# Kernel tuning notes

Hardware: AMD Instinct MI355X
Metric: run time of the kernel (lower is better)

The kernel has to match this reference:

```python
import jax, jax.numpy as jnp
import numpy as np

B, C, H, W = 16, 3, 224, 224
P = 16
DIM = 256
NL = 8
DS = 16          # d_state (mamba default)
DCONV = 4
NCLS = 1000
DI = 2 * DIM     # expand * dim
DTR = -(-DIM // 16)  # dt_rank = ceil(dim/16)
NPATCH = (H // P) * (W // P)
SEQ = NPATCH + 1


def _ln(x, g, b, eps=1e-5):
    mu = x.mean(-1, keepdims=True)
    var = ((x - mu) ** 2).mean(-1, keepdims=True)
    return (x - mu) * jax.lax.rsqrt(var + eps) * g + b


def setup_inputs() -> dict:
    key = jax.random.key(0)
    ks = jax.random.split(key, 12)
    pd = C * P * P
    s = 0.02
    return dict(
        img=jax.random.normal(ks[0], (B, C, H, W), jnp.float32),
        pe_ln1_g=jnp.ones((pd,), jnp.float32), pe_ln1_b=jnp.zeros((pd,), jnp.float32),
        pe_w=jax.random.normal(ks[1], (pd, DIM), jnp.float32) * s,
        pe_b=jnp.zeros((DIM,), jnp.float32),
        pe_ln2_g=jnp.ones((DIM,), jnp.float32), pe_ln2_b=jnp.zeros((DIM,), jnp.float32),
        pos_emb=jax.random.normal(ks[2], (1, SEQ, DIM), jnp.float32) * s,
        cls_tok=jax.random.normal(ks[3], (1, 1, DIM), jnp.float32) * s,
        ln_w=jnp.ones((NL, DIM), jnp.float32), ln_b=jnp.zeros((NL, DIM), jnp.float32),
        in_w=jax.random.normal(ks[4], (NL, DIM, 2 * DI), jnp.float32) * s,
        conv_w=jax.random.normal(ks[5], (NL, DI, DCONV), jnp.float32) * s,
        conv_b=jnp.zeros((NL, DI), jnp.float32),
        xproj_w=jax.random.normal(ks[6], (NL, DI, DTR + 2 * DS), jnp.float32) * s,
        dtproj_w=jax.random.normal(ks[7], (NL, DTR, DI), jnp.float32) * s,
        dtproj_b=jax.random.uniform(ks[8], (NL, DI), jnp.float32, -4.0, -2.0),
        A_log=jnp.log(jnp.broadcast_to(jnp.arange(1, DS + 1, dtype=jnp.float32), (NL, DI, DS))) + jnp.zeros((NL, DI, DS), jnp.float32),
        Dp=jnp.ones((NL, DI), jnp.float32),
        out_w=jax.random.normal(ks[9], (NL, DI, DIM), jnp.float32) * s,
        normf_w=jnp.ones((DIM,), jnp.float32), normf_b=jnp.zeros((DIM,), jnp.float32),
        head_w=jax.random.normal(ks[10], (DIM, NCLS), jnp.float32) * s,
        head_b=jnp.zeros((NCLS,), jnp.float32),
    )


def _mamba(x, in_w, conv_w, conv_b, xproj_w, dtproj_w, dtproj_b, A_log, Dp, out_w):
    b, L, _ = x.shape
    xz = x @ in_w                       # (b, L, 2*DI)
    xm, z = jnp.split(xz, 2, axis=-1)
    # causal depthwise conv1d (torch pads both sides then slices -> left-pad d_conv-1)
    xc = jnp.pad(xm.transpose(0, 2, 1), ((0, 0), (0, 0), (DCONV - 1, 0)))
    xc = jax.lax.conv_general_dilated(
        xc, conv_w[:, None, :], (1,), 'VALID',
        dimension_numbers=('NCH', 'OIH', 'NCH'), feature_group_count=DI)
    u = jax.nn.silu(xc + conv_b[None, :, None]).transpose(0, 2, 1)  # (b, L, DI)
    dbc = u @ xproj_w                   # (b, L, DTR+2*DS)
    dt, Bm, Cm = jnp.split(dbc, [DTR, DTR + DS], axis=-1)
    dt = jax.nn.softplus(dt @ dtproj_w + dtproj_b)  # (b, L, DI)
    A = -jnp.exp(A_log)                 # (DI, DS)

    def step(h, inp):
        dt_t, B_t, C_t, u_t = inp       # (b,DI), (b,DS), (b,DS), (b,DI)
        dA = jnp.exp(dt_t[:, :, None] * A)                 # (b, DI, DS)
        h = dA * h + (dt_t * u_t)[:, :, None] * B_t[:, None, :]
        y = jnp.einsum('bdn,bn->bd', h, C_t)
        return h, y

    h0 = jnp.zeros((b, DI, DS), x.dtype)
    xs = (dt.transpose(1, 0, 2), Bm.transpose(1, 0, 2),
          Cm.transpose(1, 0, 2), u.transpose(1, 0, 2))
    _, ys = jax.lax.scan(step, h0, xs)
    y = ys.transpose(1, 0, 2) + u * Dp  # (b, L, DI)
    y = y * jax.nn.silu(z)
    return y @ out_w                    # (b, L, DIM)


def reference(img, pe_ln1_g, pe_ln1_b, pe_w, pe_b, pe_ln2_g, pe_ln2_b, pos_emb,
              cls_tok, ln_w, ln_b, in_w, conv_w, conv_b, xproj_w, dtproj_w,
              dtproj_b, A_log, Dp, out_w, normf_w, normf_b, head_w, head_b):
    b = img.shape[0]
    h, w = H // P, W // P
    # 'b c (h p1) (w p2) -> b (h w) (p1 p2 c)'
    x = img.reshape(b, C, h, P, w, P).transpose(0, 2, 4, 3, 5, 1).reshape(b, h * w, P * P * C)
    x = _ln(x, pe_ln1_g, pe_ln1_b)
    x = x @ pe_w + pe_b
    x = _ln(x, pe_ln2_g, pe_ln2_b)
    x = jnp.concatenate([jnp.broadcast_to(cls_tok, (b, 1, DIM)), x], axis=1)
    x = x + pos_emb[:, :x.shape[1]]
    residual = None
    for i in range(NL):
        residual = x if residual is None else x + residual
        xn = _ln(residual, ln_w[i], ln_b[i])
        x = _mamba(xn, in_w[i], conv_w[i], conv_b[i], xproj_w[i],
                   dtproj_w[i], dtproj_b[i], A_log[i], Dp[i], out_w[i])
    residual = x + residual
    x = _ln(residual, normf_w, normf_b)
    x = x[:, 0]                          # pool == 'cls'
    return x @ head_w + head_b
```

## Files before the change

kernel.cpp:

```cpp
#include <hip/hip_runtime.h>
#include <math.h>

#define NB   16
#define SEQL 197
#define TB   (NB*SEQL)
#define DIMM 256
#define DI   512
#define DS   16
#define NL   8

typedef __bf16 bf16x8 __attribute__((ext_vector_type(8)));
typedef __bf16 bf16x4 __attribute__((ext_vector_type(4)));
typedef float floatx4 __attribute__((ext_vector_type(4)));

__device__ __forceinline__ void block_reduce_2(float& s1, float& s2, float* red, int tid){
  #pragma unroll
  for (int off = 32; off > 0; off >>= 1){
    s1 += __shfl_down(s1, off, 64);
    s2 += __shfl_down(s2, off, 64);
  }
  __syncthreads();
  if ((tid & 63) == 0){ red[(tid>>6)*2] = s1; red[(tid>>6)*2+1] = s2; }
  __syncthreads();
  s1 = red[0] + red[2] + red[4] + red[6];
  s2 = red[1] + red[3] + red[5] + red[7];
}

__global__ __launch_bounds__(256) void prep_weights(
    const float* __restrict__ in_w, const float* __restrict__ out_w,
    const float* __restrict__ pe_w, const float* __restrict__ xproj,
    __bf16* __restrict__ wt_in, __bf16* __restrict__ wt_out,
    __bf16* __restrict__ wt_pe, float* __restrict__ wt_xp_f)
{
  __shared__ float t[32][33];
  int bid = blockIdx.x;
  const float* src; __bf16* dst = nullptr; float* dstf = nullptr;
  int K, Nin, n0, k0;
  if (bid < 2048){
    int z = bid >> 8, tt = bid & 255;
    K = 256; Nin = 1024; n0 = (tt & 31)*32; k0 = (tt >> 5)*32;
    src = in_w  + (size_t)z*K*Nin;
    dst = wt_in + (size_t)z*K*Nin;
  } else if (bid < 3072){
    int t2 = bid - 2048; int z = t2 >> 7, tt = t2 & 127;
    K = 512; Nin = 256; n0 = (tt & 7)*32; k0 = (tt >> 3)*32;
    src = out_w  + (size_t)z*K*Nin;
    dst = wt_out + (size_t)z*K*Nin;
  } else if (bid < 3264){
    int tt = bid - 3072;
    K = 768; Nin = 256; n0 = (tt & 7)*32; k0 = (tt >> 3)*32;
    src = pe_w; dst = wt_pe;
  } else {
    int t2 = bid - 3264; int z = t2 >> 5, tt = t2 & 31;
    K = 512; Nin = 48; n0 = (tt & 1)*32; k0 = (tt >> 1)*32;
    src  = xproj + (size_t)z*K*Nin;
    dstf = wt_xp_f + (size_t)z*64*512;
  }
  int tx = threadIdx.x & 31, ty = threadIdx.x >> 5;
  #pragma unroll
  for (int j = 0; j < 4; j++){
    int n = n0 + tx;
    t[ty + j*8][tx] = (n < Nin) ? src[(size_t)(k0 + ty + j*8)*Nin + n] : 0.f;
  }
  __syncthreads();
  if (dstf){
    #pragma unroll
    for (int j = 0; j < 4; j++){
      int k = k0 + tx, c = n0 + ty + j*8;
      dstf[(size_t)(k>>2)*256 + c*4 + (k&3)] = t[tx][ty + j*8];
    }
  } else {
    #pragma unroll
    for (int j = 0; j < 4; j++)
      dst[(size_t)(n0 + ty + j*8)*K + k0 + tx] = (__bf16)t[tx][ty + j*8];
  }
}

template<int BM, int BN, int KS>
__global__ __launch_bounds__(256) void gemm_bf16(
    const __bf16* __restrict__ A, const __bf16* __restrict__ Wt,
    const float* __restrict__ bias, float* __restrict__ C, int M, int N, int K)
{
  constexpr int BK  = 32;
  constexpr int LDA = BK + 8;
  constexpr int TMW = BM/32;
  constexpr int TNW = BN/32;
  __shared__ __bf16 As[BM][LDA];
  __shared__ __bf16 Bs[BN][LDA];

  int tid  = threadIdx.x;
  int lane = tid & 63, w = tid >> 6;
  int wm = w >> 1, wn = w & 1;
  int l15 = lane & 15, quad = lane >> 4;
  int nt = blockIdx.x / KS, ks = blockIdx.x % KS;
  int bm = blockIdx.y * BM, bn = nt * BN;
  int kbeg = ks * (K / KS), kend = kbeg + (K / KS);

  floatx4 acc[TMW][TNW] = {};

  for (int k0 = kbeg; k0 < kend; k0 += BK){
    #pragma unroll
    for (int i = 0; i < BM/64; i++){
      int c = tid + i*256;
      int row = c >> 2, kc = c & 3;
      int m = bm + row;
      uint4 v = make_uint4(0,0,0,0);
      if (m < M) v = ((const uint4*)(A + (size_t)m*K + k0))[kc];
      *(uint4*)&As[row][kc*8] = v;
    }
    #pragma unroll
    for (int i = 0; i < BN/64; i++){
      int c = tid + i*256;
      int row = c >> 2, kc = c & 3;
      int n = bn + row;
      uint4 v = ((const uint4*)(Wt + (size_t)n*K + k0))[kc];
      *(uint4*)&Bs[row][kc*8] = v;
    }
    __syncthreads();
    bf16x8 af[TMW], bf[TNW];
    #pragma unroll
    for (int mi = 0; mi < TMW; mi++)
      af[mi] = *(const bf16x8*)&As[wm*(BM/2) + mi*16 + l15][quad*8];
    #pragma unroll
    for (int ni = 0; ni < TNW; ni++)
      bf[ni] = *(const bf16x8*)&Bs[wn*(BN/2) + ni*16 + l15][quad*8];
    #pragma unroll
    for (int mi = 0; mi < TMW; mi++)
      #pragma unroll
      for (int ni = 0; ni < TNW; ni++)
        acc[mi][ni] = __builtin_amdgcn_mfma_f32_16x16x32_bf16(af[mi], bf[ni], acc[mi][ni], 0, 0, 0);
    __syncthreads();
  }
  #pragma unroll
  for (int mi = 0; mi < TMW; mi++){
    #pragma unroll
    for (int ni = 0; ni < TNW; ni++){
      int col = bn + wn*(BN/2) + ni*16 + l15;
      float bv = (KS == 1 && bias) ? bias[col] : 0.f;
      #pragma unroll
      for (int r = 0; r < 4; r++){
        int row = bm + wm*(BM/2) + mi*16 + quad*4 + r;
        if (row < M){
          if (KS == 1) C[(size_t)row*N + col] = acc[mi][ni][r] + bv;
          else         atomicAdd(&C[(size_t)row*N + col], acc[mi][ni][r]);
        }
      }
    }
  }
}

template<int DO_LN>
__global__ __launch_bounds__(512) void gemm_out_fused(
    const __bf16* __restrict__ A, const __bf16* __restrict__ Wt,
    float* __restrict__ resid, __bf16* __restrict__ xn_bf,
    const float* __restrict__ g, const float* __restrict__ bta)
{
  constexpr int BK = 64, LDA = BK + 8;
  __shared__ alignas(16) char smem[(16 + 256) * LDA * sizeof(__bf16)];
  __bf16 (*As)[LDA] = (__bf16(*)[LDA])smem;
  __bf16 (*Bs)[LDA] = (__bf16(*)[LDA])(smem + 16*LDA*sizeof(__bf16));
  float  (*sy)[264] = (float(*)[264])smem;

  int tid = threadIdx.x, lane = tid & 63, w = tid >> 6;
  int l15 = lane & 15, quad = lane >> 4;
  int bm = blockIdx.x * 16;

  floatx4 acc[2] = {};
  for (int k0 = 0; k0 < 512; k0 += BK){
    if (tid < 128){
      int row = tid >> 3, kc = tid & 7;
      *(uint4*)&As[row][kc*8] = ((const uint4*)(A + (size_t)(bm+row)*512 + k0))[kc];
    }
    #pragma unroll
    for (int i = 0; i < 4; i++){
      int c = tid + i*512;
      int row = c >> 3, kc = c & 7;
      *(uint4*)&Bs[row][kc*8] = ((const uint4*)(Wt + (size_t)row*512 + k0))[kc];
    }
    __syncthreads();
    #pragma unroll
    for (int kk = 0; kk < 2; kk++){
      bf16x8 af = *(const bf16x8*)&As[l15][kk*32 + quad*8];
      #pragma unroll
      for (int ni = 0; ni < 2; ni++){
        bf16x8 bfv = *(const bf16x8*)&Bs[w*32 + ni*16 + l15][kk*32 + quad*8];
        acc[ni] = __builtin_amdgcn_mfma_f32_16x16x32_bf16(af, bfv, acc[ni], 0, 0, 0);
      }
    }
    __syncthreads();
  }
  #pragma unroll
  for (int ni = 0; ni < 2; ni++){
    int col = w*32 + ni*16 + l15;
    #pragma unroll
    for (int r = 0; r < 4; r++)
      sy[quad*4 + r][col] = acc[ni][r];
  }
  __syncthreads();
  #pragma unroll
  for (int rr = 0; rr < 2; rr++){
    int row = w*2 + rr;
    size_t base = (size_t)(bm + row)*256 + lane*4;
    float4 y4 = *(const float4*)&sy[row][lane*4];
    float4 rv = *(const float4*)&resid[base];
    float4 v;
    v.x = y4.x + rv.x; v.y = y4.y + rv.y; v.z = y4.z + rv.z; v.w = y4.w + rv.w;
    *(float4*)&resid[base] = v;
    if (DO_LN){
      float s  = v.x + v.y + v.z + v.w;
      float s2 = v.x*v.x + v.y*v.y + v.z*v.z + v.w*v.w;
      #pragma unroll
      for (int off = 1; off < 64; off <<= 1){
        s  += __shfl_xor(s,  off, 64);
        s2 += __shfl_xor(s2, off, 64);
      }
      float mu  = s * (1.f/256.f);
      float var = s2 * (1.f/256.f) - mu*mu;
      float rrq = rsqrtf(var + 1e-5f);
      float4 gv = *(const float4*)&g[lane*4];
      float4 bv = *(const float4*)&bta[lane*4];
      bf16x4 o;
      o[0] = (__bf16)((v.x - mu)*rrq*gv.x + bv.x);
      o[1] = (__bf16)((v.y - mu)*rrq*gv.y + bv.y);
      o[2] = (__bf16)((v.z - mu)*rrq*gv.z + bv.z);
      o[3] = (__bf16)((v.w - mu)*rrq*gv.w + bv.w);
      *(bf16x4*)&xn_bf[base] = o;
    }
  }
}

__global__ __launch_bounds__(256) void patch_ln1(
    const float* __restrict__ img, const float* __restrict__ g1, const float* __restrict__ b1,
    __bf16* __restrict__ xp_bf)
{
  __shared__ float red[8];
  int blk = blockIdx.x;
  int b = blk / 196, p = blk % 196;
  int hh = p / 14, ww = p % 14;
  int tid = threadIdx.x;

  float v[3]; float s = 0.f, s2 = 0.f;
  #pragma unroll
  for (int i = 0; i < 3; i++){
    int e  = tid + i*256;
    int c  = e % 3;
    int p2 = (e/3) % 16;
    int p1 = e / 48;
    float val = img[((b*3 + c)*224 + hh*16 + p1)*224 + ww*16 + p2];
    v[i] = val; s += val; s2 += val*val;
  }
  block_reduce_2(s, s2, red, tid);
  float mu = s * (1.f/768.f);
  float var = s2 * (1.f/768.f) - mu*mu;
  float rr = rsqrtf(var + 1e-5f);
  #pragma unroll
  for (int i = 0; i < 3; i++){
    int e = tid + i*256;
    xp_bf[(size_t)blk*768 + e] = (__bf16)((v[i] - mu) * rr * g1[e] + b1[e]);
  }
}

__global__ __launch_bounds__(256) void ln2_cls_pos(
    const float* __restrict__ pemb, const float* __restrict__ g2, const float* __restrict__ b2,
    const float* __restrict__ pos, const float* __restrict__ cls,
    float* __restrict__ resid,
    const float* __restrict__ g0, const float* __restrict__ b0,
    __bf16* __restrict__ xn_bf)
{
  __shared__ float red[8];
  int blk = blockIdx.x;
  int b = blk / SEQL, l = blk % SEQL;
  int tid = threadIdx.x;
  float o;
  if (l == 0){
    o = cls[tid] + pos[tid];
  } else {
    int p = l - 1;
    float v = pemb[(size_t)(b*196 + p)*256 + tid];
    float s = v, s2 = v*v;
    block_reduce_2(s, s2, red, tid);
    float mu = s * (1.f/256.f);
    float var = s2 * (1.f/256.f) - mu*mu;
    float rr = rsqrtf(var + 1e-5f);
    o = (v - mu) * rr * g2[tid] + b2[tid] + pos[l*256 + tid];
  }
  size_t idx = (size_t)blk*256 + tid;
  resid[idx] = o;
  float s = o, s2 = o*o;
  block_reduce_2(s, s2, red, tid);
  float mu = s * (1.f/256.f);
  float var = s2 * (1.f/256.f) - mu*mu;
  float rr = rsqrtf(var + 1e-5f);
  xn_bf[idx] = (__bf16)((o - mu) * rr * g0[tid] + b0[tid]);
}

__global__ __launch_bounds__(256) void conv_xproj(
    const float* __restrict__ xz, const float* __restrict__ cw, const float* __restrict__ cb,
    const float* __restrict__ wxp,
    float* __restrict__ u, float* __restrict__ dbc)
{
  __shared__ float s_u[8][512];
  __shared__ float s_acc[4][8][64];
  int tid = threadIdx.x;
  int t0 = blockIdx.x * 8;

  int d = (tid & 127) * 4;
  float4 w0 = *(const float4*)&cw[(d+0)*4];
  float4 w1 = *(const float4*)&cw[(d+1)*4];
  float4 w2 = *(const float4*)&cw[(d+2)*4];
  float4 w3 = *(const float4*)&cw[(d+3)*4];
  float4 cbv = *(const float4*)&cb[d];
  const float4 z4 = make_float4(0.f,0.f,0.f,0.f);
  #pragma unroll
  for (int j = 0; j < 4; j++){
    int tl = (tid >> 7)*4 + j;
    int t = t0 + tl;
    int l = t % SEQL;
    float4 x0 = *(const float4*)&xz[(size_t)t*1024 + d];
    float4 x1 = (l>=1) ? *(const float4*)&xz[(size_t)(t-1)*1024 + d] : z4;
    float4 x2 = (l>=2) ? *(const float4*)&xz[(size_t)(t-2)*1024 + d] : z4;
    float4 x3 = (l>=3) ? *(const float4*)&xz[(size_t)(t-3)*1024 + d] : z4;
    float4 r = cbv;
    r.x += x3.x*w0.x + x2.x*w0.y + x1.x*w0.z + x0.x*w0.w;
    r.y += x3.y*w1.x + x2.y*w1.y + x1.y*w1.z + x0.y*w1.w;
    r.z += x3.z*w2.x + x2.z*w2.y + x1.z*w2.z + x0.z*w2.w;
    r.w += x3.w*w3.x + x2.w*w3.y + x1.w*w3.z + x0.w*w3.w;
    r.x *= 1.f/(1.f + __expf(-r.x));
    r.y *= 1.f/(1.f + __expf(-r.y));
    r.z *= 1.f/(1.f + __expf(-r.z));
    r.w *= 1.f/(1.f + __expf(-r.w));
    *(float4*)&u[(size_t)t*512 + d] = r;
    *(float4*)&s_u[tl][d] = r;
  }
  __syncthreads();

  int col = tid & 63, sl = tid >> 6;
  const float4* wp4 = (const float4*)wxp + (size_t)sl*32*64 + col;
  float a[8] = {};
  #pragma unroll 4
  for (int k4 = 0; k4 < 32; k4++){
    float4 wv = wp4[(size_t)k4*64];
    #pragma unroll
    for (int t = 0; t < 8; t++){
      float4 v = *(const float4*)&s_u[t][sl*128 + k4*4];
      a[t] += wv.x*v.x + wv.y*v.y + wv.z*v.z + wv.w*v.w;
    }
  }
  #pragma unroll
  for (int t = 0; t < 8; t++) s_acc[sl][t][col] = a[t];
  __syncthreads();
  #pragma unroll
  for (int j = 0; j < 2; j++){
    int p = tid + j*256;
    int tok = p >> 6, c2 = p & 63;
    if (c2 < 48){
      float v = s_acc[0][tok][c2] + s_acc[1][tok][c2]
              + s_acc[2][tok][c2] + s_acc[3][tok][c2];
      dbc[(size_t)(t0 + tok)*64 + c2] = v;
    }
  }
}

#define SCT 32
#define NCH ((SEQL + SCT - 1)/SCT)
#define NDL 8
__global__ __launch_bounds__(128) void scan_kernel(
    const float* __restrict__ u, const float* __restrict__ dbc,
    const float* __restrict__ xz, const float* __restrict__ A_log, const float* __restrict__ Dp,
    const float* __restrict__ dtw, const float* __restrict__ dtb,
    __bf16* __restrict__ yg_bf)
{
  __shared__ float s_D [16][36];
  __shared__ float s_B [16][36];
  __shared__ float s_C [16][36];
  __shared__ float s_u [NDL][36];
  __shared__ float s_z [NDL][36];
  __shared__ float s_dt[NDL][36];
  __shared__ float s_yp[SCT][NDL][20];
  __shared__ float s_dp[NDL];

  int tid = threadIdx.x;
  int n = tid & 15, dl = tid >> 4;
  int b = blockIdx.x >> 6, dg = blockIdx.x & 63;
  int d0 = dg * NDL;
  const size_t base = (size_t)b * SEQL;

  float A = -__expf(A_log[(d0+dl)*DS + n]);
  float h = 0.f;
  if (tid < NDL) s_dp[tid] = Dp[d0 + tid];
  int cch = tid & 7;
  float wc[16];
  #pragma unroll
  for (int k = 0; k < 16; k++) wc[k] = dtw[k*512 + d0 + cch];
  float dtbv = dtb[d0 + cch];

  float r_u[2], r_z[2], r_db[12];
  auto load_regs = [&](int c){
    #pragma unroll
    for (int i = 0; i < 2; i++){
      int v = tid + i*128;
      int tg = c*SCT + (v>>3); if (tg > SEQL-1) tg = SEQL-1;
      size_t t = base + tg;
      r_u[i] = u [t*512 + d0 + (v&7)];
      r_z[i] = xz[t*1024 + 512 + d0 + (v&7)];
    }
    #pragma unroll
    for (int s = 0; s < 3; s++)
      #pragma unroll
      for (int i = 0; i < 4; i++){
        int v = tid + i*128;
        int tg = c*SCT + (v>>4); if (tg > SEQL-1) tg = SEQL-1;
        r_db[s*4+i] = dbc[(base + tg)*64 + s*16 + (v&15)];
      }
  };
  auto write_DBC = [&](){
    #pragma unroll
    for (int i = 0; i < 4; i++){
      int v = tid + i*128;
      s_D[v&15][v>>4] = r_db[0+i];
      s_B[v&15][v>>4] = r_db[4+i];
      s_C[v&15][v>>4] = r_db[8+i];
    }
  };
  auto write_UZ = [&](){
    #pragma unroll
    for (int i = 0; i < 2; i++){
      int v = tid + i*128;
      s_u[v&7][v>>3] = r_u[i];
      s_z[v&7][v>>3] = r_z[i];
    }
  };
  auto compute_dt = [&](){
    #pragma unroll
    for (int i = 0; i < 2; i++){
      int tl = (tid >> 3) + i*16;
      float acc = dtbv;
      #pragma unroll
      for (int k = 0; k < 16; k++) acc += s_D[k][tl] * wc[k];
      s_dt[cch][tl] = (acc > 20.f) ? acc : log1pf(__expf(acc));
    }
  };

  load_regs(0);
  write_DBC();
  write_UZ();
  __syncthreads();
  compute_dt();
  __syncthreads();

  for (int c = 0; c < NCH; c++){
    if (c + 1 < NCH) load_regs(c+1);

    float4 dt4, u4, B4, C4;
    #pragma unroll
    for (int tl = 0; tl < SCT; tl++){
      if ((tl & 3) == 0){
        dt4 = *(const float4*)&s_dt[dl][tl];
        u4  = *(const float4*)&s_u [dl][tl];
        B4  = *(const float4*)&s_B [n][tl];
        C4  = *(const float4*)&s_C [n][tl];
      }
      float dtv = ((float*)&dt4)[tl&3];
      float uv  = ((float*)&u4 )[tl&3];
      float Bv  = ((float*)&B4 )[tl&3];
      float Cv  = ((float*)&C4 )[tl&3];
      h = __expf(dtv * A) * h + (dtv * uv) * Bv;
      s_yp[tl][dl][n] = h * Cv;
    }
    __syncthreads();

    if (c + 1 < NCH) write_DBC();

    #pragma unroll
    for (int j = 0; j < 2; j++){
      int p = tid + j*128;
      int tl = p >> 3, dr = p & 7;
      float4 a0 = *(const float4*)&s_yp[tl][dr][0];
      float4 a1 = *(const float4*)&s_yp[tl][dr][4];
      float4 a2 = *(const float4*)&s_yp[tl][dr][8];
      float4 a3 = *(const float4*)&s_yp[tl][dr][12];
      float yv = ((a0.x+a0.y)+(a0.z+a0.w)) + ((a1.x+a1.y)+(a1.z+a1.w))
               + ((a2.x+a2.y)+(a2.z+a2.w)) + ((a3.x+a3.y)+(a3.z+a3.w));
      int tg = c*SCT + tl;
      if (tg < SEQL){
        float uv = s_u[dr][tl];
        float zv = s_z[dr][tl];
        float sg = 1.f / (1.f + __expf(-zv));
        yg_bf[(base + tg)*512 + d0 + dr] = (__bf16)((yv + uv*s_dp[dr]) * zv * sg);
      }
    }
    __syncthreads();

    if (c + 1 < NCH){
      write_UZ();
      compute_dt();
      __syncthreads();
    }
  }
}

__global__ __launch_bounds__(256) void final_ln(
    const float* __restrict__ resid,
    const float* __restrict__ g, const float* __restrict__ bta, float* __restrict__ xs_g)
{
  __shared__ float red[8];
  int b = blockIdx.x, tid = threadIdx.x;
  size_t idx = (size_t)b*SEQL*256 + tid;
  float r = resid[idx];
  float s = r, s2 = r*r;
  block_reduce_2(s, s2, red, tid);
  float mu = s * (1.f/256.f);
  float var = s2 * (1.f/256.f) - mu*mu;
  float rr = rsqrtf(var + 1e-5f);
  xs_g[b*256 + tid] = (r - mu) * rr * g[tid] + bta[tid];
}

__global__ __launch_bounds__(256) void head_gemm(
    const float* __restrict__ xs_g, const float* __restrict__ head_w,
    const float* __restrict__ head_b, float* __restrict__ out)
{
  __shared__ float xs[16][256];
  int tid = threadIdx.x;
  #pragma unroll
  for (int i = 0; i < 16; i++) ((float*)xs)[tid + i*256] = xs_g[tid + i*256];
  __syncthreads();
  int nl = tid & 31, bq = tid >> 5;
  int nn = blockIdx.x*32 + nl;
  if (nn >= 1000) return;
  float acc0 = 0.f, acc1 = 0.f;
  #pragma unroll 8
  for (int k = 0; k < 256; k++){
    float w = head_w[k*1000 + nn];
    acc0 += xs[bq][k]   * w;
    acc1 += xs[bq+8][k] * w;
  }
  float hb = head_b[nn];
  out[(size_t)bq*1000 + nn]     = acc0 + hb;
  out[(size_t)(bq+8)*1000 + nn] = acc1 + hb;
}

extern "C" void kernel_launch(void* const* d_in, const int* in_sizes, int n_in,
                              void* d_out, int out_size, void* d_ws, size_t ws_size,
                              hipStream_t stream) {
  const float* img   = (const float*)d_in[0];
  const float* ln1g  = (const float*)d_in[1];
  const float* ln1b  = (const float*)d_in[2];
  const float* pe_w  = (const float*)d_in[3];
  const float* pe_b  = (const float*)d_in[4];
  const float* ln2g  = (const float*)d_in[5];
  const float* ln2b  = (const float*)d_in[6];
  const float* pos   = (const float*)d_in[7];
  const float* cls   = (const float*)d_in[8];
  const float* ln_w  = (const float*)d_in[9];
  const float* ln_b  = (const float*)d_in[10];
  const float* in_w  = (const float*)d_in[11];
  const float* conv_w= (const float*)d_in[12];
  const float* conv_b= (const float*)d_in[13];
  const float* xproj = (const float*)d_in[14];
  const float* dtw   = (const float*)d_in[15];
  const float* dtb   = (const float*)d_in[16];
  const float* A_log = (const float*)d_in[17];
  const float* Dp    = (const float*)d_in[18];
  const float* out_w = (const float*)d_in[19];
  const float* nfw   = (const float*)d_in[20];
  const float* nfb   = (const float*)d_in[21];
  const float* head_w= (const float*)d_in[22];
  const float* head_b= (const float*)d_in[23];
  float* out = (float*)d_out;

  float* ws = (float*)d_ws;
  float* resid = ws;  ws += (size_t)TB*DIMM;
  float* xz    = ws;  ws += (size_t)TB*2*DI;
  float* u     = ws;  ws += (size_t)TB*DI;
  float* dbc   = ws;  ws += (size_t)TB*64;
  float* xs_g  = ws;  ws += (size_t)NB*DIMM;
  float* wt_xp_f = ws; ws += (size_t)NL*64*512;
  __bf16* xn_bf = (__bf16*)ws;  ws += (size_t)TB*DIMM/2;
  __bf16* yg_bf = (__bf16*)ws;  ws += (size_t)TB*DI/2;
  __bf16* wt_in = (__bf16*)ws;  ws += (size_t)NL*1024*256/2;
  __bf16* wt_out= (__bf16*)ws;  ws += (size_t)NL*256*512/2;
  __bf16* wt_pe = (__bf16*)ws;  ws += (size_t)256*768/2;
  __bf16* xp_bf = (__bf16*)xz;
  float*  pemb  = u;

  prep_weights<<<3520, 256, 0, stream>>>(in_w, out_w, pe_w, xproj,
                                          wt_in, wt_out, wt_pe, wt_xp_f);

  patch_ln1<<<NB*196, 256, 0, stream>>>(img, ln1g, ln1b, xp_bf);
  gemm_bf16<64,64,1><<<dim3(256/64, 3136/64), 256, 0, stream>>>(
      xp_bf, wt_pe, pe_b, pemb, 3136, 256, 768);
  ln2_cls_pos<<<NB*SEQL, 256, 0, stream>>>(pemb, ln2g, ln2b, pos, cls,
                                           resid, ln_w, ln_b, xn_bf);

  for (int i = 0; i < NL; i++){
    gemm_bf16<64,128,1><<<dim3(1024/128, (TB+63)/64), 256, 0, stream>>>(
        xn_bf, wt_in + (size_t)i*1024*256, nullptr, xz, TB, 1024, 256);
    conv_xproj<<<TB/8, 256, 0, stream>>>(
        xz, conv_w + i*DI*4, conv_b + i*DI, wt_xp_f + (size_t)i*64*512, u, dbc);
    scan_kernel<<<NB*64, 128, 0, stream>>>(
        u, dbc, xz, A_log + i*DI*DS, Dp + i*DI, dtw + i*16*DI, dtb + i*DI, yg_bf);
    if (i < NL-1)
      gemm_out_fused<1><<<TB/16, 512, 0, stream>>>(
          yg_bf, wt_out + (size_t)i*256*512, resid, xn_bf,
          ln_w + (i+1)*DIMM, ln_b + (i+1)*DIMM);
    else
      gemm_out_fused<0><<<TB/16, 512, 0, stream>>>(
          yg_bf, wt_out + (size_t)i*256*512, resid, nullptr, nullptr, nullptr);
  }
  final_ln<<<NB, 256, 0, stream>>>(resid, nfw, nfb, xs_g);
  head_gemm<<<(1000+31)/32, 256, 0, stream>>>(xs_g, head_w, head_b, out);
}
```

Baseline: 658.8 us.

## Fuse next layer's in-projection GEMM into out-projection + LayerNorm kernel

The out-projection kernel now keeps the LayerNorm-ed 16-row tile in LDS and immediately multiplies it by the next layer's in_w (1024 columns), writing xz directly. This drops the separate in-projection GEMM launch and the xn_bf global round trip for layers 1..7. The cost is that each 16-row block reads the full 256x1024 bf16 in_w from global/L2 without LDS staging, and the small M tile (16) gives poor weight reuse compared with the 64x128 tiled GEMM.

Result: slower. 689.2 us (+4.6%).

```diff
diff --git a/kernel.cpp b/kernel.cpp
--- a/kernel.cpp
+++ b/kernel.cpp
@@ -149,17 +149,18 @@
   }
 }
 
-template<int DO_LN>
-__global__ __launch_bounds__(512) void gemm_out_fused(
-    const __bf16* __restrict__ A, const __bf16* __restrict__ Wt,
-    float* __restrict__ resid, __bf16* __restrict__ xn_bf,
-    const float* __restrict__ g, const float* __restrict__ bta)
+__global__ __launch_bounds__(512) void gemm_out_in(
+    const __bf16* __restrict__ A, const __bf16* __restrict__ Wout,
+    float* __restrict__ resid,
+    const float* __restrict__ g, const float* __restrict__ bta,
+    const __bf16* __restrict__ Win, float* __restrict__ xz)
 {
   constexpr int BK = 64, LDA = BK + 8;
   __shared__ alignas(16) char smem[(16 + 256) * LDA * sizeof(__bf16)];
   __bf16 (*As)[LDA] = (__bf16(*)[LDA])smem;
   __bf16 (*Bs)[LDA] = (__bf16(*)[LDA])(smem + 16*LDA*sizeof(__bf16));
   float  (*sy)[264] = (float(*)[264])smem;
+  __shared__ __bf16 xn_lds[16][264];
 
   int tid = threadIdx.x, lane = tid & 63, w = tid >> 6;
   int l15 = lane & 15, quad = lane >> 4;
@@ -175,7 +176,7 @@
     for (int i = 0; i < 4; i++){
       int c = tid + i*512;
       int row = c >> 3, kc = c & 7;
-      *(uint4*)&Bs[row][kc*8] = ((const uint4*)(Wt + (size_t)row*512 + k0))[kc];
+      *(uint4*)&Bs[row][kc*8] = ((const uint4*)(Wout + (size_t)row*512 + k0))[kc];
     }
     __syncthreads();
     #pragma unroll
@@ -206,26 +207,103 @@
     float4 v;
     v.x = y4.x + rv.x; v.y = y4.y + rv.y; v.z = y4.z + rv.z; v.w = y4.w + rv.w;
     *(float4*)&resid[base] = v;
-    if (DO_LN){
-      float s  = v.x + v.y + v.z + v.w;
-      float s2 = v.x*v.x + v.y*v.y + v.z*v.z + v.w*v.w;
+    float s  = v.x + v.y + v.z + v.w;
+    float s2 = v.x*v.x + v.y*v.y + v.z*v.z + v.w*v.w;
+    #pragma unroll
+    for (int off = 1; off < 64; off <<= 1){
+      s  += __shfl_xor(s,  off, 64);
+      s2 += __shfl_xor(s2, off, 64);
+    }
+    float mu  = s * (1.f/256.f);
+    float var = s2 * (1.f/256.f) - mu*mu;
+    float rrq = rsqrtf(var + 1e-5f);
+    float4 gv = *(const float4*)&g[lane*4];
+    float4 bv = *(const float4*)&bta[lane*4];
+    bf16x4 o;
+    o[0] = (__bf16)((v.x - mu)*rrq*gv.x + bv.x);
+    o[1] = (__bf16)((v.y - mu)*rrq*gv.y + bv.y);
+    o[2] = (__bf16)((v.z - mu)*rrq*gv.z + bv.z);
+    o[3] = (__bf16)((v.w - mu)*rrq*gv.w + bv.w);
+    *(bf16x4*)&xn_lds[row][lane*4] = o;
+  }
+  __syncthreads();
+
+  floatx4 acc2[8] = {};
+  const __bf16* wb = Win + ((size_t)(w*128 + l15))*256 + quad*8;
+  for (int k0 = 0; k0 < 256; k0 += 32){
+    bf16x8 af = *(const bf16x8*)&xn_lds[l15][k0 + quad*8];
+    #pragma unroll
+    for (int nt = 0; nt < 8; nt++){
+      bf16x8 bfv = *(const bf16x8*)(wb + (size_t)nt*16*256 + k0);
+      acc2[nt] = __builtin_amdgcn_mfma_f32_16x16x32_bf16(af, bfv, acc2[nt], 0, 0, 0);
+    }
+  }
+  #pragma unroll
+  for (int nt = 0; nt < 8; nt++){
+    int col = w*128 + nt*16 + l15;
+    #pragma unroll
+    for (int r = 0; r < 4; r++){
+      int row = quad*4 + r;
+      xz[(size_t)(bm+row)*1024 + col] = acc2[nt][r];
+    }
+  }
+}
+
+__global__ __launch_bounds__(512) void gemm_out_last(
+    const __bf16* __restrict__ A, const __bf16* __restrict__ Wt,
+    float* __restrict__ resid)
+{
+  constexpr int BK = 64, LDA = BK + 8;
+  __shared__ alignas(16) char smem[(16 + 256) * LDA * sizeof(__bf16)];
+  __bf16 (*As)[LDA] = (__bf16(*)[LDA])smem;
+  __bf16 (*Bs)[LDA] = (__bf16(*)[LDA])(smem + 16*LDA*sizeof(__bf16));
+  float  (*sy)[264] = (float(*)[264])smem;
+
+  int tid = threadIdx.x, lane = tid & 63, w = tid >> 6;
+  int l15 = lane & 15, quad = lane >> 4;
+  int bm = blockIdx.x * 16;
+
+  floatx4 acc[2] = {};
+  for (int k0 = 0; k0 < 512; k0 += BK){
+    if (tid < 128){
+      int row = tid >> 3, kc = tid & 7;
+      *(uint4*)&As[row][kc*8] = ((const uint4*)(A + (size_t)(bm+row)*512 + k0))[kc];
+    }
+    #pragma unroll
+    for (int i = 0; i < 4; i++){
+      int c = tid + i*512;
+      int row = c >> 3, kc = c & 7;
+      *(uint4*)&Bs[row][kc*8] = ((const uint4*)(Wt + (size_t)row*512 + k0))[kc];
+    }
+    __syncthreads();
+    #pragma unroll
+    for (int kk = 0; kk < 2; kk++){
+      bf16x8 af = *(const bf16x8*)&As[l15][kk*32 + quad*8];
       #pragma unroll
-      for (int off = 1; off < 64; off <<= 1){
-        s  += __shfl_xor(s,  off, 64);
-        s2 += __shfl_xor(s2, off, 64);
+      for (int ni = 0; ni < 2; ni++){
+        bf16x8 bfv = *(const bf16x8*)&Bs[w*32 + ni*16 + l15][kk*32 + quad*8];
+        acc[ni] = __builtin_amdgcn_mfma_f32_16x16x32_bf16(af, bfv, acc[ni], 0, 0, 0);
       }
-      float mu  = s * (1.f/256.f);
-      float var = s2 * (1.f/256.f) - mu*mu;
-      float rrq = rsqrtf(var + 1e-5f);
-      float4 gv = *(const float4*)&g[lane*4];
-      float4 bv = *(const float4*)&bta[lane*4];
-      bf16x4 o;
-      o[0] = (__bf16)((v.x - mu)*rrq*gv.x + bv.x);
-      o[1] = (__bf16)((v.y - mu)*rrq*gv.y + bv.y);
-      o[2] = (__bf16)((v.z - mu)*rrq*gv.z + bv.z);
-      o[3] = (__bf16)((v.w - mu)*rrq*gv.w + bv.w);
-      *(bf16x4*)&xn_bf[base] = o;
-    }
+    }
+    __syncthreads();
+  }
+  #pragma unroll
+  for (int ni = 0; ni < 2; ni++){
+    int col = w*32 + ni*16 + l15;
+    #pragma unroll
+    for (int r = 0; r < 4; r++)
+      sy[quad*4 + r][col] = acc[ni][r];
+  }
+  __syncthreads();
+  #pragma unroll
+  for (int rr = 0; rr < 2; rr++){
+    int row = w*2 + rr;
+    size_t base = (size_t)(bm + row)*256 + lane*4;
+    float4 y4 = *(const float4*)&sy[row][lane*4];
+    float4 rv = *(const float4*)&resid[base];
+    float4 v;
+    v.x = y4.x + rv.x; v.y = y4.y + rv.y; v.z = y4.z + rv.z; v.w = y4.w + rv.w;
+    *(float4*)&resid[base] = v;
   }
 }
 
@@ -591,21 +669,22 @@
       xp_bf, wt_pe, pe_b, pemb, 3136, 256, 768);
   ln2_cls_pos<<<NB*SEQL, 256, 0, stream>>>(pemb, ln2g, ln2b, pos, cls,
                                            resid, ln_w, ln_b, xn_bf);
+  gemm_bf16<64,128,1><<<dim3(1024/128, (TB+63)/64), 256, 0, stream>>>(
+      xn_bf, wt_in, nullptr, xz, TB, 1024, 256);
 
   for (int i = 0; i < NL; i++){
-    gemm_bf16<64,128,1><<<dim3(1024/128, (TB+63)/64), 256, 0, stream>>>(
-        xn_bf, wt_in + (size_t)i*1024*256, nullptr, xz, TB, 1024, 256);
     conv_xproj<<<TB/8, 256, 0, stream>>>(
         xz, conv_w + i*DI*4, conv_b + i*DI, wt_xp_f + (size_t)i*64*512, u, dbc);
     scan_kernel<<<NB*64, 128, 0, stream>>>(
         u, dbc, xz, A_log + i*DI*DS, Dp + i*DI, dtw + i*16*DI, dtb + i*DI, yg_bf);
     if (i < NL-1)
-      gemm_out_fused<1><<<TB/16, 512, 0, stream>>>(
-          yg_bf, wt_out + (size_t)i*256*512, resid, xn_bf,
-          ln_w + (i+1)*DIMM, ln_b + (i+1)*DIMM);
+      gemm_out_in<<<TB/16, 512, 0, stream>>>(
+          yg_bf, wt_out + (size_t)i*256*512, resid,
+          ln_w + (i+1)*DIMM, ln_b + (i+1)*DIMM,
+          wt_in + (size_t)(i+1)*1024*256, xz);
     else
-      gemm_out_fused<0><<<TB/16, 512, 0, stream>>>(
-          yg_bf, wt_out + (size_t)i*256*512, resid, nullptr, nullptr, nullptr);
+      gemm_out_last<<<TB/16, 512, 0, stream>>>(
+          yg_bf, wt_out + (size_t)i*256*512, resid);
   }
   final_ln<<<NB, 256, 0, stream>>>(resid, nfw, nfb, xs_g);
   head_gemm<<<(1000+31)/32, 256, 0, stream>>>(xs_g, head_w, head_b, out);
```
